# Performance work log

Hardware: AMD Instinct MI355X
Metric: run time of the kernel (lower is better)

The kernel has to match this reference:

```python
import jax, jax.numpy as jnp
import numpy as np

N, S, E = 8, 2048, 512
H, D = 8, 64            # heads, head_dim
P = 16                  # num_persistent
ALIBI_ALPHA = 1.0
START_I = 0


def setup_inputs() -> dict:
    key = jax.random.key(0)
    ks = jax.random.split(key, 12)
    inp = {
        "values": jax.random.normal(ks[0], (N, S, E), jnp.float32),
        "keys": jax.random.normal(ks[1], (N, S, E), jnp.float32),
        "queries": jax.random.normal(ks[2], (N, S, E), jnp.float32),
        "mask": jax.random.randint(ks[3], (N, 1, S, S), 0, 2, jnp.int32),
        # per-head-dim projections (torch Linear, no bias): weight shape (out, in)
        "Wv": jax.random.normal(ks[4], (D, D), jnp.float32) / np.sqrt(D),
        "Wk": jax.random.normal(ks[5], (D, D), jnp.float32) / np.sqrt(D),
        "Wq": jax.random.normal(ks[6], (D, D), jnp.float32) / np.sqrt(D),
        "Wo": jax.random.normal(ks[7], (E, E), jnp.float32) / np.sqrt(E),
        "bo": jnp.zeros((E,), jnp.float32),
        # talking-heads 1x1 conv weights, squeezed to (H_out, H_in)
        "pre_th": jax.random.normal(ks[8], (H, H), jnp.float32) / np.sqrt(H),
        "post_th": jax.random.normal(ks[9], (H, H), jnp.float32) / np.sqrt(H),
        # persistent memory tokens (P, H, D)
        "pk": jax.random.normal(ks[10], (P, H, D), jnp.float32) * 0.1,
        "pv": jax.random.normal(ks[11], (P, H, D), jnp.float32) * 0.1,
    }
    return inp


def reference(values, keys, queries, mask, Wv, Wk, Wq, Wo, bo, pre_th, post_th, pk, pv):
    n, q_len, e = queries.shape
    k_len = keys.shape[1]
    h, d = pk.shape[1], pk.shape[2]

    # split heads: [n, s, h, d]
    v = values.reshape(n, -1, h, d)
    k = keys.reshape(n, -1, h, d)
    q = queries.reshape(n, -1, h, d)

    # per-head-dim linear projections (torch: x @ W.T)
    v = jnp.einsum('nshd,ed->nshe', v, Wv)
    k = jnp.einsum('nshd,ed->nshe', k, Wk)
    q = jnp.einsum('nshd,ed->nshe', q, Wq)

    # append persistent memory tokens along key/value sequence dim
    p = pk.shape[0]
    k = jnp.concatenate([k, jnp.broadcast_to(pk[None], (n, p, h, d))], axis=1)
    v = jnp.concatenate([v, jnp.broadcast_to(pv[None], (n, p, h, d))], axis=1)

    # energy: [n, h, q, k_len + p]
    energy = jnp.einsum('nqhd,nkhd->nhqk', q, k)

    # ALiBi bias: -|i - j| * slope_h, zero bias on persistent slots
    slopes = 2.0 ** (-ALIBI_ALPHA * (jnp.arange(1, h + 1, dtype=jnp.float32) + START_I))
    t_q = jnp.arange(q_len)
    t_k = jnp.arange(k_len)
    dist = jnp.abs(t_q[:, None] - t_k[None, :]).astype(jnp.float32)  # [q, k]
    alibi = -dist[None, None] * slopes[None, :, None, None]          # [1, h, q, k]
    alibi = jnp.pad(alibi, ((0, 0), (0, 0), (0, 0), (0, p)))
    energy = energy + alibi

    # pre-softmax talking heads (1x1 conv over head channel)
    energy = jnp.einsum('ij,njqk->niqk', pre_th, energy)

    # mask (pad persistent slots with 1 = keep)
    mask_p = jnp.pad(mask, ((0, 0), (0, 0), (0, 0), (0, p)), constant_values=1)
    energy = jnp.where(mask_p == 0, jnp.float32(-1e4), energy)

    attn = jax.nn.softmax(energy / jnp.sqrt(jnp.float32(e)), axis=3)

    # post-softmax talking heads
    attn = jnp.einsum('ij,njqk->niqk', post_th, attn)

    out = jnp.einsum('nhql,nlhd->nqhd', attn, v).reshape(n, q_len, e)
    out = out @ Wo.T + bo
    return out
```

## Files before the change

### kernel.cpp

```cpp
#include <hip/hip_runtime.h>

#define N_ 8
#define S_ 2048
#define E_ 512
#define KL_ 2064
#define NTT_ 65
#define VTSZ 1064960
#define SCALE2 0.063758723f
#define NEGBIG -700.0f

typedef unsigned short u16;
typedef unsigned int u32;
typedef __attribute__((ext_vector_type(2))) float f32x2;
typedef __attribute__((ext_vector_type(4))) float f32x4;
typedef __attribute__((ext_vector_type(4))) short bf16x4;
typedef __attribute__((ext_vector_type(8))) short bf16x8;

__device__ __forceinline__ u16 f2bf(float x) {
  u32 u = __float_as_uint(x);
  u32 r = (u + 0x7FFFu + ((u >> 16) & 1u)) >> 16;
  return (u16)r;
}

__device__ __forceinline__ float exp2_fast(float x) {
  float r;
  asm("v_exp_f32 %0, %1" : "=v"(r) : "v"(x));
  return r;
}

__device__ __forceinline__ f32x4 mfma16(bf16x4 a, bf16x4 b, f32x4 c) {
#if __has_builtin(__builtin_amdgcn_mfma_f32_16x16x16bf16_1k)
  return __builtin_amdgcn_mfma_f32_16x16x16bf16_1k(a, b, c, 0, 0, 0);
#else
  f32x4 d;
  asm("v_mfma_f32_16x16x16_bf16 %0, %1, %2, %3" : "=v"(d) : "v"(a), "v"(b), "v"(c));
  return d;
#endif
}

__device__ __forceinline__ void gload_lds16(const void* g, void* l) {
  __builtin_amdgcn_global_load_lds((const __attribute__((address_space(1))) unsigned int*)g,
                                   (__attribute__((address_space(3))) unsigned int*)l, 16, 0, 0);
}

__global__ __launch_bounds__(256) void maskpack_kernel(const int* __restrict__ mask,
                                                       u32* __restrict__ bm) {
  const int t = threadIdx.x;
  const int w = t >> 6, lane = t & 63;
  const int blk = blockIdx.x;
  const int n = blk >> 9;
  const int qrow = ((blk & 511) << 2) + w;
  const int* row = mask + ((size_t)n * S_ + qrow) * S_;
  __shared__ u32 tl[4][64];
  u32 myword = 0;
  #pragma unroll 4
  for (int k = 0; k < 32; ++k) {
    int v = row[k * 64 + lane];
    unsigned long long b = __ballot(v != 0);
    if ((lane >> 1) == k) myword = (lane & 1) ? (u32)(b >> 32) : (u32)b;
  }
  tl[w][lane] = myword;
  __syncthreads();
  const int qq = t & 3, wi = t >> 2;
  const int qb = ((blk & 511) << 2) + qq;
  bm[((size_t)n * 64 + wi) * S_ + qb] = tl[qq][wi];
}

__global__ __launch_bounds__(256, 2) void proj_kernel(
    const float* __restrict__ V_, const float* __restrict__ K_, const float* __restrict__ Q_,
    const float* __restrict__ Wv, const float* __restrict__ Wk, const float* __restrict__ Wq,
    u16* __restrict__ Kp, u16* __restrict__ Qp, u16* __restrict__ VT) {
  __shared__ u16 xt[64 * 512];
  __shared__ u16 wt[64 * 64];
  const int tz = blockIdx.y;
  const float* X = (tz == 0) ? V_ : (tz == 1) ? K_ : Q_;
  const float* W = (tz == 0) ? Wv : (tz == 1) ? Wk : Wq;
  const int t = threadIdx.x, lane = t & 63, w = t >> 6, g = lane >> 4, li = lane & 15;
  const int rb = blockIdx.x * 64;
  const int nn = rb >> 11, sb = rb & 2047;

  for (int c = t; c < 512; c += 256) {
    int r = c >> 3, s = c & 7;
    float4 a = *(const float4*)&W[r * 64 + s * 8];
    float4 b = *(const float4*)&W[r * 64 + s * 8 + 4];
    bf16x8 v = {(short)f2bf(a.x), (short)f2bf(a.y), (short)f2bf(a.z), (short)f2bf(a.w),
                (short)f2bf(b.x), (short)f2bf(b.y), (short)f2bf(b.z), (short)f2bf(b.w)};
    *(bf16x8*)&wt[r * 64 + ((s ^ (r & 7)) * 8)] = v;
  }
  for (int c = t; c < 4096; c += 256) {
    int r = c >> 6, s = c & 63;
    const float* src = &X[(size_t)(rb + r) * 512 + s * 8];
    float4 a = *(const float4*)src;
    float4 b = *(const float4*)(src + 4);
    bf16x8 v = {(short)f2bf(a.x), (short)f2bf(a.y), (short)f2bf(a.z), (short)f2bf(a.w),
                (short)f2bf(b.x), (short)f2bf(b.y), (short)f2bf(b.z), (short)f2bf(b.w)};
    *(bf16x8*)&xt[r * 512 + ((s ^ (r & 7)) * 8)] = v;
  }
  __syncthreads();

  bf16x8 fx[8][2];
  #pragma unroll
  for (int h = 0; h < 8; ++h)
    #pragma unroll
    for (int dh = 0; dh < 2; ++dh) {
      int row = w * 16 + li;
      fx[h][dh] = *(const bf16x8*)&xt[row * 512 + (((h * 8 + dh * 4 + g) ^ (row & 7)) * 8)];
    }
  bf16x8 fw[4][2];
  #pragma unroll
  for (int c = 0; c < 4; ++c)
    #pragma unroll
    for (int dh = 0; dh < 2; ++dh) {
      int row = c * 16 + li;
      fw[c][dh] = *(const bf16x8*)&wt[row * 64 + (((dh * 4 + g) ^ (row & 7)) * 8)];
    }

  f32x4 C[8][4];
  #pragma unroll
  for (int h = 0; h < 8; ++h)
    #pragma unroll
    for (int c = 0; c < 4; ++c) C[h][c] = (f32x4){0.f, 0.f, 0.f, 0.f};

  if (tz == 0) {
    #pragma unroll
    for (int h = 0; h < 8; ++h)
      #pragma unroll
      for (int dh = 0; dh < 2; ++dh)
        #pragma unroll
        for (int c = 0; c < 4; ++c)
          C[h][c] = __builtin_amdgcn_mfma_f32_16x16x32_bf16(fw[c][dh], fx[h][dh], C[h][c], 0, 0, 0);
    #pragma unroll
    for (int h = 0; h < 8; ++h)
      #pragma unroll
      for (int c = 0; c < 4; ++c)
        #pragma unroll
        for (int r = 0; r < 4; ++r) {
          int e = h * 64 + c * 16 + g * 4 + r;
          int l = sb + w * 16 + li;
          VT[(((size_t)nn * 65 + (l >> 5)) * 512 + e) * 32 + (l & 31)] = f2bf(C[h][c][r]);
        }
  } else {
    #pragma unroll
    for (int h = 0; h < 8; ++h)
      #pragma unroll
      for (int dh = 0; dh < 2; ++dh)
        #pragma unroll
        for (int c = 0; c < 4; ++c)
          C[h][c] = __builtin_amdgcn_mfma_f32_16x16x32_bf16(fx[h][dh], fw[c][dh], C[h][c], 0, 0, 0);
    #pragma unroll
    for (int h = 0; h < 8; ++h)
      #pragma unroll
      for (int c = 0; c < 4; ++c)
        #pragma unroll
        for (int r = 0; r < 4; ++r) {
          int e = h * 64 + c * 16 + li;
          u16 val = f2bf(C[h][c][r]);
          if (tz == 2) Qp[(size_t)(rb + w * 16 + g * 4 + r) * 512 + e] = val;
          else Kp[((size_t)nn * KL_ + sb + w * 16 + g * 4 + r) * 512 + e] = val;
        }
  }
}

__global__ __launch_bounds__(256) void persist_kernel(const float* __restrict__ pk,
                                                      const float* __restrict__ pv,
                                                      u16* __restrict__ Kp, u16* __restrict__ VT) {
  int id = blockIdx.x * 256 + threadIdx.x;
  if (id < 65536) {
    int n = id >> 13, p = (id >> 9) & 15, e = id & 511;
    Kp[((size_t)n * KL_ + S_ + p) * 512 + e] = f2bf(pk[p * 512 + e]);
  } else {
    int rem = id - 65536;
    int n = rem >> 14, p = (rem >> 9) & 31, e = rem & 511;
    u16 val = (p < 16) ? f2bf(pv[p * 512 + e]) : (u16)0;
    VT[(((size_t)n * 65 + 64) * 512 + e) * 32 + p] = val;
  }
}

__global__ __launch_bounds__(512, 2) void attn_kernel(
    const u16* __restrict__ Qp, const u16* __restrict__ Kp, const u16* __restrict__ VT,
    const u32* __restrict__ bm, const float* __restrict__ pre_th,
    const float* __restrict__ post_th, u16* __restrict__ Ohb) {
  __shared__ __align__(16) char smem[151552];
  u16* KtB = (u16*)smem;
  u16* VtB = (u16*)(smem + 65536);
  u32* mlds = (u32*)(smem + 131072);
  float* Zbuf = (float*)(smem + 147456);

  const int t = threadIdx.x, lane = t & 63, w = t >> 6, g = lane >> 4, li = lane & 15;
  const int qw = w & 3, lh = w >> 2;
  const int bid = blockIdx.x;
  const int n = bid & 7;
  const int q0 = (bid >> 3) * 64;
  const int myq = q0 + qw * 16 + li;
  const float myq_f = (float)myq;

  const u16* Kbase = Kp + (size_t)n * KL_ * 512;
  const u16* Vbase = VT + (size_t)n * VTSZ;

  #define STAGE_K(buf, tile) {                                                          \
    _Pragma("unroll")                                                                   \
    for (int i_ = 0; i_ < 4; ++i_) {                                                    \
      int row_ = w + i_ * 8;                                                            \
      gload_lds16(Kbase + (size_t)((tile) * 32 + row_) * 512 + ((lane ^ (row_ & 7)) * 8),\
                  KtB + (buf) * 16384 + row_ * 512);                                    \
    } }
  #define STAGE_V(buf, tile) {                                                          \
    _Pragma("unroll")                                                                   \
    for (int i_ = 0; i_ < 4; ++i_) {                                                    \
      int c_ = t + i_ * 512;                                                            \
      int e_ = c_ >> 2, q16_ = c_ & 3;                                                  \
      gload_lds16(Vbase + (size_t)(tile) * 16384 + e_ * 32 + ((q16_ ^ (e_ & 3)) * 8),   \
                  VtB + (buf) * 16384 + (i_ * 512 + w * 64) * 8);                       \
    } }

  for (int idx = t; idx < 4096; idx += 512)
    mlds[idx] = bm[((size_t)n * 64 + (idx >> 6)) * S_ + q0 + (idx & 63)];

  bf16x8 qf[8][2];
  {
    const u16* qrow = Qp + (size_t)(n * S_ + myq) * 512;
    #pragma unroll
    for (int h = 0; h < 8; ++h)
      #pragma unroll
      for (int dh = 0; dh < 2; ++dh)
        qf[h][dh] = *(const bf16x8*)(qrow + h * 64 + dh * 32 + g * 8);
  }
  float nms[8];
  #pragma unroll
  for (int i = 0; i < 8; ++i) {
    float a = 0.f;
    #pragma unroll
    for (int j = 0; j < 8; ++j) a += pre_th[i * 8 + j] * exp2f(-(float)(j + 1));
    nms[i] = -a * SCALE2;
  }

  float Zr[8];
  #pragma unroll
  for (int i = 0; i < 8; ++i) Zr[i] = 0.f;

  STAGE_K(0, 0)
  __syncthreads();

  for (int tt = 0; tt < NTT_; ++tt) {
    if (tt + 1 < NTT_) STAGE_K((tt + 1) & 1, tt + 1)
    const u16* kb = KtB + (tt & 1) * 16384;
    f32x4 C[8];
    #pragma unroll
    for (int h = 0; h < 8; ++h) C[h] = (f32x4){0.f, 0.f, 0.f, 0.f};
    #pragma unroll
    for (int h = 0; h < 8; ++h)
      #pragma unroll
      for (int dh = 0; dh < 2; ++dh) {
        bf16x8 a = *(const bf16x8*)(kb + (lh * 16 + li) * 512 + (((h * 8 + dh * 4 + g) ^ (li & 7)) * 8));
        C[h] = __builtin_amdgcn_mfma_f32_16x16x32_bf16(a, qf[h][dh], C[h], 0, 0, 0);
      }
    u32 mbits;
    float dist[4];
    const int l0 = tt * 32 + lh * 16 + g * 4;
    if (tt < 64) {
      mbits = (mlds[tt * 64 + qw * 16 + li] >> (lh * 16 + g * 4)) & 0xFu;
      #pragma unroll
      for (int r = 0; r < 4; ++r) dist[r] = fabsf(myq_f - (float)(l0 + r));
    } else {
      mbits = (lh == 0) ? 0xFu : 0u;
      #pragma unroll
      for (int r = 0; r < 4; ++r) dist[r] = 0.f;
    }
    f32x2 accl[8], acch[8];
    #pragma unroll
    for (int i = 0; i < 8; ++i) { accl[i] = (f32x2){0.f, 0.f}; acch[i] = (f32x2){0.f, 0.f}; }
    #pragma unroll
    for (int j = 0; j < 8; ++j) {
      f32x2 elo = {C[j].x, C[j].y}, ehi = {C[j].z, C[j].w};
      #pragma unroll
      for (int i = 0; i < 8; ++i) {
        float p = pre_th[i * 8 + j];
        accl[i] += p * elo; acch[i] += p * ehi;
      }
    }
    const bool al = (tt < 64);
    #pragma unroll
    for (int i = 0; i < 8; ++i) {
      float t0 = fmaf(accl[i].x, SCALE2, -64.f);
      float t1 = fmaf(accl[i].y, SCALE2, -64.f);
      float t2 = fmaf(acch[i].x, SCALE2, -64.f);
      float t3 = fmaf(acch[i].y, SCALE2, -64.f);
      if (al) {
        t0 = fmaf(dist[0], nms[i], t0); t1 = fmaf(dist[1], nms[i], t1);
        t2 = fmaf(dist[2], nms[i], t2); t3 = fmaf(dist[3], nms[i], t3);
      }
      t0 = (mbits & 1u) ? t0 : NEGBIG; t1 = (mbits & 2u) ? t1 : NEGBIG;
      t2 = (mbits & 4u) ? t2 : NEGBIG; t3 = (mbits & 8u) ? t3 : NEGBIG;
      Zr[i] += (exp2_fast(t0) + exp2_fast(t1)) + (exp2_fast(t2) + exp2_fast(t3));
    }
    __syncthreads();
  }

  STAGE_K(0, 0)
  STAGE_V(0, 0)

  #pragma unroll
  for (int i = 0; i < 8; ++i) {
    Zr[i] += __shfl_xor(Zr[i], 16);
    Zr[i] += __shfl_xor(Zr[i], 32);
  }
  if (lane < 16) {
    #pragma unroll
    for (int i = 0; i < 8; ++i) Zbuf[(lh * 64 + qw * 16 + li) * 8 + i] = Zr[i];
  }
  __syncthreads();
  float nm1[8];
  #pragma unroll
  for (int i = 0; i < 8; ++i) {
    float zt = Zbuf[(qw * 16 + li) * 8 + i] + Zbuf[(64 + qw * 16 + li) * 8 + i];
    nm1[i] = -(64.f + __log2f(zt));
  }

  f32x4 O[8][4];
  #pragma unroll
  for (int o = 0; o < 8; ++o)
    #pragma unroll
    for (int dc = 0; dc < 4; ++dc) O[o][dc] = (f32x4){0.f, 0.f, 0.f, 0.f};

  const int cloff = (((lh * 2 + (g >> 1)) ^ (li & 3)) * 8) + (g & 1) * 4;

  for (int tt = 0; tt < NTT_; ++tt) {
    if (tt + 1 < NTT_) { STAGE_K((tt + 1) & 1, tt + 1) STAGE_V((tt + 1) & 1, tt + 1) }
    const u16* kb = KtB + (tt & 1) * 16384;
    const u16* vb = VtB + (tt & 1) * 16384;
    f32x4 C[8];
    #pragma unroll
    for (int h = 0; h < 8; ++h) C[h] = (f32x4){0.f, 0.f, 0.f, 0.f};
    #pragma unroll
    for (int h = 0; h < 8; ++h)
      #pragma unroll
      for (int dh = 0; dh < 2; ++dh) {
        bf16x8 a = *(const bf16x8*)(kb + (lh * 16 + li) * 512 + (((h * 8 + dh * 4 + g) ^ (li & 7)) * 8));
        C[h] = __builtin_amdgcn_mfma_f32_16x16x32_bf16(a, qf[h][dh], C[h], 0, 0, 0);
      }
    u32 mbits;
    float dist[4];
    const int l0 = tt * 32 + lh * 16 + g * 4;
    if (tt < 64) {
      mbits = (mlds[tt * 64 + qw * 16 + li] >> (lh * 16 + g * 4)) & 0xFu;
      #pragma unroll
      for (int r = 0; r < 4; ++r) dist[r] = fabsf(myq_f - (float)(l0 + r));
    } else {
      mbits = (lh == 0) ? 0xFu : 0u;
      #pragma unroll
      for (int r = 0; r < 4; ++r) dist[r] = 0.f;
    }
    f32x2 accl[8], acch[8];
    #pragma unroll
    for (int i = 0; i < 8; ++i) { accl[i] = (f32x2){0.f, 0.f}; acch[i] = (f32x2){0.f, 0.f}; }
    #pragma unroll
    for (int j = 0; j < 8; ++j) {
      f32x2 elo = {C[j].x, C[j].y}, ehi = {C[j].z, C[j].w};
      #pragma unroll
      for (int i = 0; i < 8; ++i) {
        float p = pre_th[i * 8 + j];
        accl[i] += p * elo; acch[i] += p * ehi;
      }
    }
    const bool al = (tt < 64);
    f32x2 ppl[8], pph[8];
    #pragma unroll
    for (int i = 0; i < 8; ++i) {
      float t0 = fmaf(accl[i].x, SCALE2, nm1[i]);
      float t1 = fmaf(accl[i].y, SCALE2, nm1[i]);
      float t2 = fmaf(acch[i].x, SCALE2, nm1[i]);
      float t3 = fmaf(acch[i].y, SCALE2, nm1[i]);
      if (al) {
        t0 = fmaf(dist[0], nms[i], t0); t1 = fmaf(dist[1], nms[i], t1);
        t2 = fmaf(dist[2], nms[i], t2); t3 = fmaf(dist[3], nms[i], t3);
      }
      t0 = (mbits & 1u) ? t0 : NEGBIG; t1 = (mbits & 2u) ? t1 : NEGBIG;
      t2 = (mbits & 4u) ? t2 : NEGBIG; t3 = (mbits & 8u) ? t3 : NEGBIG;
      ppl[i] = (f32x2){exp2_fast(t0), exp2_fast(t1)};
      pph[i] = (f32x2){exp2_fast(t2), exp2_fast(t3)};
    }
    f32x2 pol[8], poh[8];
    #pragma unroll
    for (int o = 0; o < 8; ++o) { pol[o] = (f32x2){0.f, 0.f}; poh[o] = (f32x2){0.f, 0.f}; }
    #pragma unroll
    for (int i = 0; i < 8; ++i) {
      #pragma unroll
      for (int o = 0; o < 8; ++o) {
        float c = post_th[o * 8 + i];
        pol[o] += c * ppl[i]; poh[o] += c * pph[i];
      }
    }
    #pragma unroll
    for (int o = 0; o < 8; ++o) {
      bf16x4 pa = {(short)f2bf(pol[o].x), (short)f2bf(pol[o].y),
                   (short)f2bf(poh[o].x), (short)f2bf(poh[o].y)};
      #pragma unroll
      for (int dc = 0; dc < 4; ++dc) {
        int e = o * 64 + dc * 16 + li;
        bf16x4 b = *(const bf16x4*)(vb + e * 32 + cloff);
        O[o][dc] = mfma16(pa, b, O[o][dc]);
      }
    }
    __syncthreads();
  }

  float* ep = (float*)smem;
  if (lh == 1) {
    #pragma unroll
    for (int o = 0; o < 8; ++o)
      #pragma unroll
      for (int dc = 0; dc < 4; ++dc)
        *(f32x4*)&ep[qw * 8192 + ((o * 4 + dc) * 64 + li * 4 + g) * 4] = O[o][dc];
  }
  __syncthreads();
  if (lh == 0) {
    u16* dst = Ohb + (size_t)(n * S_ + q0 + qw * 16) * 512;
    #pragma unroll
    for (int o = 0; o < 8; ++o)
      #pragma unroll
      for (int dc = 0; dc < 4; ++dc) {
        f32x4 oth = *(const f32x4*)&ep[qw * 8192 + ((o * 4 + dc) * 64 + li * 4 + g) * 4];
        f32x4 v = O[o][dc] + oth;
        int e = o * 64 + dc * 16 + li;
        #pragma unroll
        for (int r = 0; r < 4; ++r) dst[(size_t)(g * 4 + r) * 512 + e] = f2bf(v[r]);
      }
  }
  #undef STAGE_K
  #undef STAGE_V
}

__global__ __launch_bounds__(256) void out_proj_kernel(
    const u16* __restrict__ Ohb, const float* __restrict__ Wo,
    const float* __restrict__ bo, float* __restrict__ out) {
  __shared__ __align__(16) u16 As[2][128 * 32];
  __shared__ __align__(16) u16 Bs[2][128 * 32];
  const int t = threadIdx.x, lane = t & 63, w = t >> 6, g = lane >> 4, li = lane & 15;
  const int wq = w & 1, wp = w >> 1;
  const int r0 = blockIdx.y * 128, c0 = blockIdx.x * 128;

  #define STAGE_A(buf, ks) {                                                  \
    _Pragma("unroll")                                                         \
    for (int i_ = 0; i_ < 2; ++i_) {                                          \
      int c_ = t + i_ * 256;                                                  \
      gload_lds16(Ohb + (size_t)(r0 + (c_ >> 2)) * 512 + (ks) + (c_ & 3) * 8, \
                  &As[buf][(i_ * 256 + w * 64) * 8]);                         \
    } }
  #define STAGE_B(buf, ks) {                                                  \
    _Pragma("unroll")                                                         \
    for (int i_ = 0; i_ < 2; ++i_) {                                          \
      int c_ = t + i_ * 256;                                                  \
      const float* s_ = &Wo[(size_t)(c0 + (c_ >> 2)) * 512 + (ks) + (c_ & 3) * 8]; \
      float4 a_ = *(const float4*)s_;                                         \
      float4 b_ = *(const float4*)(s_ + 4);                                   \
      bf16x8 v_ = {(short)f2bf(a_.x), (short)f2bf(a_.y), (short)f2bf(a_.z), (short)f2bf(a_.w), \
                   (short)f2bf(b_.x), (short)f2bf(b_.y), (short)f2bf(b_.z), (short)f2bf(b_.w)}; \
      *(bf16x8*)&Bs[buf][c_ * 8] = v_;                                        \
    } }

  f32x4 acc[4][4];
  #pragma unroll
  for (int m = 0; m < 4; ++m)
    #pragma unroll
    for (int nn = 0; nn < 4; ++nn) acc[m][nn] = (f32x4){0.f, 0.f, 0.f, 0.f};

  STAGE_A(0, 0)
  STAGE_B(0, 0)
  __syncthreads();
  for (int s = 0; s < 16; ++s) {
    if (s + 1 < 16) { STAGE_A((s + 1) & 1, (s + 1) * 32) STAGE_B((s + 1) & 1, (s + 1) * 32) }
    const u16* ab = As[s & 1];
    const u16* bb = Bs[s & 1];
    bf16x8 af[4], bf[4];
    #pragma unroll
    for (int m = 0; m < 4; ++m) af[m] = *(const bf16x8*)(ab + (wp * 64 + m * 16 + li) * 32 + g * 8);
    #pragma unroll
    for (int nn = 0; nn < 4; ++nn) bf[nn] = *(const bf16x8*)(bb + (wq * 64 + nn * 16 + li) * 32 + g * 8);
    #pragma unroll
    for (int m = 0; m < 4; ++m)
      #pragma unroll
      for (int nn = 0; nn < 4; ++nn)
        acc[m][nn] = __builtin_amdgcn_mfma_f32_16x16x32_bf16(af[m], bf[nn], acc[m][nn], 0, 0, 0);
    __syncthreads();
  }
  #pragma unroll
  for (int nn = 0; nn < 4; ++nn) {
    int col = c0 + wq * 64 + nn * 16 + li;
    float bv = bo[col];
    #pragma unroll
    for (int m = 0; m < 4; ++m)
      #pragma unroll
      for (int r = 0; r < 4; ++r)
        out[(size_t)(r0 + wp * 64 + m * 16 + g * 4 + r) * 512 + col] = acc[m][nn][r] + bv;
  }
  #undef STAGE_A
  #undef STAGE_B
}

extern "C" void kernel_launch(void* const* d_in, const int* in_sizes, int n_in,
                              void* d_out, int out_size, void* d_ws, size_t ws_size,
                              hipStream_t stream) {
  const float* values  = (const float*)d_in[0];
  const float* keys    = (const float*)d_in[1];
  const float* queries = (const float*)d_in[2];
  const int*   mask    = (const int*)d_in[3];
  const float* Wv      = (const float*)d_in[4];
  const float* Wk      = (const float*)d_in[5];
  const float* Wq      = (const float*)d_in[6];
  const float* Wo      = (const float*)d_in[7];
  const float* bo      = (const float*)d_in[8];
  const float* pre_th  = (const float*)d_in[9];
  const float* post_th = (const float*)d_in[10];
  const float* pk      = (const float*)d_in[11];
  const float* pv      = (const float*)d_in[12];

  char* ws = (char*)d_ws;
  u16*  Qp  = (u16*)ws;
  u16*  Kp  = (u16*)(ws + 16777216);
  u16*  VT  = (u16*)(ws + 33685504);
  u16*  Ohb = (u16*)(ws + 50724864);
  u32*  bm  = (u32*)(ws + 67502080);

  hipLaunchKernelGGL(maskpack_kernel, dim3(4096), dim3(256), 0, stream, mask, bm);
  hipLaunchKernelGGL(proj_kernel, dim3(256, 3), dim3(256), 0, stream,
                     values, keys, queries, Wv, Wk, Wq, Kp, Qp, VT);
  hipLaunchKernelGGL(persist_kernel, dim3(768), dim3(256), 0, stream, pk, pv, Kp, VT);
  hipLaunchKernelGGL(attn_kernel, dim3(256), dim3(512), 0, stream,
                     Qp, Kp, VT, bm, pre_th, post_th, Ohb);
  hipLaunchKernelGGL(out_proj_kernel, dim3(4, 128), dim3(256), 0, stream,
                     Ohb, Wo, bo, (float*)d_out);
}
```

Measured before the change: 986.3 us.

## Read K, V and mask directly from global memory instead of LDS staging

Drops the double-buffered LDS staging of K and V tiles and the per-block mask preload. Each wave now loads its K rows, V fragments and mask words straight from global memory (relying on L1/L2), which removes the per-tile __syncthreads barriers. It also wraps the MFMA sections in s_setprio raises. The risk is more global and cache traffic and exposed load latency, because there is no explicit prefetch. Uncoalesced 8-byte V fragment loads may also cost more than the LDS reads they replace.

```diff
diff --git a/kernel.cpp b/kernel.cpp
--- a/kernel.cpp
+++ b/kernel.cpp
@@ -180,11 +180,8 @@
     const u16* __restrict__ Qp, const u16* __restrict__ Kp, const u16* __restrict__ VT,
     const u32* __restrict__ bm, const float* __restrict__ pre_th,
     const float* __restrict__ post_th, u16* __restrict__ Ohb) {
-  __shared__ __align__(16) char smem[151552];
-  u16* KtB = (u16*)smem;
-  u16* VtB = (u16*)(smem + 65536);
-  u32* mlds = (u32*)(smem + 131072);
-  float* Zbuf = (float*)(smem + 147456);
+  __shared__ __align__(16) float ep[32768];
+  __shared__ float Zbuf[2 * 64 * 8];
 
   const int t = threadIdx.x, lane = t & 63, w = t >> 6, g = lane >> 4, li = lane & 15;
   const int qw = w & 3, lh = w >> 2;
@@ -196,25 +193,7 @@
 
   const u16* Kbase = Kp + (size_t)n * KL_ * 512;
   const u16* Vbase = VT + (size_t)n * VTSZ;
-
-  #define STAGE_K(buf, tile) {                                                          \
-    _Pragma("unroll")                                                                   \
-    for (int i_ = 0; i_ < 4; ++i_) {                                                    \
-      int row_ = w + i_ * 8;                                                            \
-      gload_lds16(Kbase + (size_t)((tile) * 32 + row_) * 512 + ((lane ^ (row_ & 7)) * 8),\
-                  KtB + (buf) * 16384 + row_ * 512);                                    \
-    } }
-  #define STAGE_V(buf, tile) {                                                          \
-    _Pragma("unroll")                                                                   \
-    for (int i_ = 0; i_ < 4; ++i_) {                                                    \
-      int c_ = t + i_ * 512;                                                            \
-      int e_ = c_ >> 2, q16_ = c_ & 3;                                                  \
-      gload_lds16(Vbase + (size_t)(tile) * 16384 + e_ * 32 + ((q16_ ^ (e_ & 3)) * 8),   \
-                  VtB + (buf) * 16384 + (i_ * 512 + w * 64) * 8);                       \
-    } }
-
-  for (int idx = t; idx < 4096; idx += 512)
-    mlds[idx] = bm[((size_t)n * 64 + (idx >> 6)) * S_ + q0 + (idx & 63)];
+  const u32* bmq = bm + (size_t)n * 64 * S_ + q0 + qw * 16 + li;
 
   bf16x8 qf[8][2];
   {
@@ -238,34 +217,27 @@
   #pragma unroll
   for (int i = 0; i < 8; ++i) Zr[i] = 0.f;
 
-  STAGE_K(0, 0)
-  __syncthreads();
-
   for (int tt = 0; tt < NTT_; ++tt) {
-    if (tt + 1 < NTT_) STAGE_K((tt + 1) & 1, tt + 1)
-    const u16* kb = KtB + (tt & 1) * 16384;
+    const u16* Krow = Kbase + ((size_t)tt * 32 + lh * 16 + li) * 512;
+    u32 word = (tt < 64) ? bmq[(size_t)tt * S_] : ((lh == 0) ? 0xFFFFFFFFu : 0u);
     f32x4 C[8];
     #pragma unroll
     for (int h = 0; h < 8; ++h) C[h] = (f32x4){0.f, 0.f, 0.f, 0.f};
-    #pragma unroll
-    for (int h = 0; h < 8; ++h)
-      #pragma unroll
-      for (int dh = 0; dh < 2; ++dh) {
-        bf16x8 a = *(const bf16x8*)(kb + (lh * 16 + li) * 512 + (((h * 8 + dh * 4 + g) ^ (li & 7)) * 8));
-        C[h] = __builtin_amdgcn_mfma_f32_16x16x32_bf16(a, qf[h][dh], C[h], 0, 0, 0);
-      }
-    u32 mbits;
+    __builtin_amdgcn_s_setprio(1);
+    #pragma unroll
+    for (int h = 0; h < 8; ++h) {
+      bf16x8 a0 = *(const bf16x8*)(Krow + (h * 8 + g) * 8);
+      bf16x8 a1 = *(const bf16x8*)(Krow + (h * 8 + 4 + g) * 8);
+      C[h] = __builtin_amdgcn_mfma_f32_16x16x32_bf16(a0, qf[h][0], C[h], 0, 0, 0);
+      C[h] = __builtin_amdgcn_mfma_f32_16x16x32_bf16(a1, qf[h][1], C[h], 0, 0, 0);
+    }
+    __builtin_amdgcn_s_setprio(0);
+    const u32 mbits = (word >> (lh * 16 + g * 4)) & 0xFu;
+    const bool al = (tt < 64);
     float dist[4];
     const int l0 = tt * 32 + lh * 16 + g * 4;
-    if (tt < 64) {
-      mbits = (mlds[tt * 64 + qw * 16 + li] >> (lh * 16 + g * 4)) & 0xFu;
-      #pragma unroll
-      for (int r = 0; r < 4; ++r) dist[r] = fabsf(myq_f - (float)(l0 + r));
-    } else {
-      mbits = (lh == 0) ? 0xFu : 0u;
-      #pragma unroll
-      for (int r = 0; r < 4; ++r) dist[r] = 0.f;
-    }
+    #pragma unroll
+    for (int r = 0; r < 4; ++r) dist[r] = al ? fabsf(myq_f - (float)(l0 + r)) : 0.f;
     f32x2 accl[8], acch[8];
     #pragma unroll
     for (int i = 0; i < 8; ++i) { accl[i] = (f32x2){0.f, 0.f}; acch[i] = (f32x2){0.f, 0.f}; }
@@ -278,7 +250,6 @@
         accl[i] += p * elo; acch[i] += p * ehi;
       }
     }
-    const bool al = (tt < 64);
     #pragma unroll
     for (int i = 0; i < 8; ++i) {
       float t0 = fmaf(accl[i].x, SCALE2, -64.f);
@@ -293,11 +264,7 @@
       t2 = (mbits & 4u) ? t2 : NEGBIG; t3 = (mbits & 8u) ? t3 : NEGBIG;
       Zr[i] += (exp2_fast(t0) + exp2_fast(t1)) + (exp2_fast(t2) + exp2_fast(t3));
     }
-    __syncthreads();
-  }
-
-  STAGE_K(0, 0)
-  STAGE_V(0, 0)
+  }
 
   #pragma unroll
   for (int i = 0; i < 8; ++i) {
@@ -322,34 +289,28 @@
     #pragma unroll
     for (int dc = 0; dc < 4; ++dc) O[o][dc] = (f32x4){0.f, 0.f, 0.f, 0.f};
 
-  const int cloff = (((lh * 2 + (g >> 1)) ^ (li & 3)) * 8) + (g & 1) * 4;
-
   for (int tt = 0; tt < NTT_; ++tt) {
-    if (tt + 1 < NTT_) { STAGE_K((tt + 1) & 1, tt + 1) STAGE_V((tt + 1) & 1, tt + 1) }
-    const u16* kb = KtB + (tt & 1) * 16384;
-    const u16* vb = VtB + (tt & 1) * 16384;
+    const u16* Krow = Kbase + ((size_t)tt * 32 + lh * 16 + li) * 512;
+    const u16* Vtile = Vbase + (size_t)tt * 16384;
+    u32 word = (tt < 64) ? bmq[(size_t)tt * S_] : ((lh == 0) ? 0xFFFFFFFFu : 0u);
     f32x4 C[8];
     #pragma unroll
     for (int h = 0; h < 8; ++h) C[h] = (f32x4){0.f, 0.f, 0.f, 0.f};
-    #pragma unroll
-    for (int h = 0; h < 8; ++h)
-      #pragma unroll
-      for (int dh = 0; dh < 2; ++dh) {
-        bf16x8 a = *(const bf16x8*)(kb + (lh * 16 + li) * 512 + (((h * 8 + dh * 4 + g) ^ (li & 7)) * 8));
-        C[h] = __builtin_amdgcn_mfma_f32_16x16x32_bf16(a, qf[h][dh], C[h], 0, 0, 0);
-      }
-    u32 mbits;
+    __builtin_amdgcn_s_setprio(1);
+    #pragma unroll
+    for (int h = 0; h < 8; ++h) {
+      bf16x8 a0 = *(const bf16x8*)(Krow + (h * 8 + g) * 8);
+      bf16x8 a1 = *(const bf16x8*)(Krow + (h * 8 + 4 + g) * 8);
+      C[h] = __builtin_amdgcn_mfma_f32_16x16x32_bf16(a0, qf[h][0], C[h], 0, 0, 0);
+      C[h] = __builtin_amdgcn_mfma_f32_16x16x32_bf16(a1, qf[h][1], C[h], 0, 0, 0);
+    }
+    __builtin_amdgcn_s_setprio(0);
+    const u32 mbits = (word >> (lh * 16 + g * 4)) & 0xFu;
+    const bool al = (tt < 64);
     float dist[4];
     const int l0 = tt * 32 + lh * 16 + g * 4;
-    if (tt < 64) {
-      mbits = (mlds[tt * 64 + qw * 16 + li] >> (lh * 16 + g * 4)) & 0xFu;
-      #pragma unroll
-      for (int r = 0; r < 4; ++r) dist[r] = fabsf(myq_f - (float)(l0 + r));
-    } else {
-      mbits = (lh == 0) ? 0xFu : 0u;
-      #pragma unroll
-      for (int r = 0; r < 4; ++r) dist[r] = 0.f;
-    }
+    #pragma unroll
+    for (int r = 0; r < 4; ++r) dist[r] = al ? fabsf(myq_f - (float)(l0 + r)) : 0.f;
     f32x2 accl[8], acch[8];
     #pragma unroll
     for (int i = 0; i < 8; ++i) { accl[i] = (f32x2){0.f, 0.f}; acch[i] = (f32x2){0.f, 0.f}; }
@@ -362,7 +323,6 @@
         accl[i] += p * elo; acch[i] += p * ehi;
       }
     }
-    const bool al = (tt < 64);
     f32x2 ppl[8], pph[8];
     #pragma unroll
     for (int i = 0; i < 8; ++i) {
@@ -390,6 +350,7 @@
         pol[o] += c * ppl[i]; poh[o] += c * pph[i];
       }
     }
+    __builtin_amdgcn_s_setprio(1);
     #pragma unroll
     for (int o = 0; o < 8; ++o) {
       bf16x4 pa = {(short)f2bf(pol[o].x), (short)f2bf(pol[o].y),
@@ -397,14 +358,13 @@
       #pragma unroll
       for (int dc = 0; dc < 4; ++dc) {
         int e = o * 64 + dc * 16 + li;
-        bf16x4 b = *(const bf16x4*)(vb + e * 32 + cloff);
+        bf16x4 b = *(const bf16x4*)(Vtile + e * 32 + lh * 16 + g * 4);
         O[o][dc] = mfma16(pa, b, O[o][dc]);
       }
     }
-    __syncthreads();
-  }
-
-  float* ep = (float*)smem;
+    __builtin_amdgcn_s_setprio(0);
+  }
+
   if (lh == 1) {
     #pragma unroll
     for (int o = 0; o < 8; ++o)
@@ -426,8 +386,6 @@
         for (int r = 0; r < 4; ++r) dst[(size_t)(g * 4 + r) * 512 + e] = f2bf(v[r]);
       }
   }
-  #undef STAGE_K
-  #undef STAGE_V
 }
 
 __global__ __launch_bounds__(256) void out_proj_kernel(
```

Result: slower. 1.252 ms (+27.0%).
